# Kernel optimization log

Measured on AMD Instinct MI355X. Metric: run time of the kernel, lower is better.

## Reference

```python
import jax, jax.numpy as jnp
import numpy as np

N_NODES = 262144
N_EDGES = 4194304
N_GRAPHS = 1024
IN_DIM = 10
HIDDEN = 32


def setup_inputs() -> dict:
    key = jax.random.key(0)
    ks = jax.random.split(key, 8)
    x = jax.random.normal(ks[0], (N_NODES, IN_DIM), dtype=jnp.float32)
    edge_index = jax.random.randint(ks[1], (2, N_EDGES), 0, N_NODES, dtype=jnp.int64)
    batch = jnp.sort(jax.random.randint(ks[2], (N_NODES,), 0, N_GRAPHS, dtype=jnp.int64))
    W1 = jax.random.normal(ks[3], (IN_DIM, HIDDEN), dtype=jnp.float32) * (1.0 / np.sqrt(IN_DIM))
    b1 = jnp.zeros((HIDDEN,), dtype=jnp.float32)
    W2 = jax.random.normal(ks[4], (HIDDEN, HIDDEN), dtype=jnp.float32) * (1.0 / np.sqrt(HIDDEN))
    b2 = jnp.zeros((HIDDEN,), dtype=jnp.float32)
    Wlin = jax.random.normal(ks[5], (HIDDEN, 1), dtype=jnp.float32) * (1.0 / np.sqrt(HIDDEN))
    blin = jnp.zeros((1,), dtype=jnp.float32)
    return {"x": x, "edge_index": edge_index, "batch": batch,
            "W1": W1, "b1": b1, "W2": W2, "b2": b2, "Wlin": Wlin, "blin": blin}


def _gcn_norm(edge_index, num_nodes):
    # PyG GCNConv default: add self-loops, symmetric normalization.
    loop = jnp.arange(num_nodes, dtype=edge_index.dtype)
    src = jnp.concatenate([edge_index[0], loop])
    dst = jnp.concatenate([edge_index[1], loop])
    deg = jax.ops.segment_sum(jnp.ones_like(dst, dtype=jnp.float32), dst,
                              num_segments=num_nodes)
    dinv = jnp.where(deg > 0, jax.lax.rsqrt(deg), 0.0)
    norm = dinv[src] * dinv[dst]  # [E+N]
    return src, dst, norm


def _gcn_conv(x, W, b, src, dst, norm, num_nodes):
    h = x @ W                              # [N, out]
    msg = h[src] * norm[:, None]           # gather + scale  [E+N, out]
    out = jax.ops.segment_sum(msg, dst, num_segments=num_nodes)  # scatter-add
    return out + b


def reference(x, edge_index, batch, W1, b1, W2, b2, Wlin, blin):
    n = x.shape[0]
    src, dst, norm = _gcn_norm(edge_index, n)
    h = jax.nn.relu(_gcn_conv(x, W1, b1, src, dst, norm, n))
    h = jax.nn.relu(_gcn_conv(h, W2, b2, src, dst, norm, n))
    # global_mean_pool over graph ids
    sums = jax.ops.segment_sum(h, batch, num_segments=N_GRAPHS)
    cnt = jax.ops.segment_sum(jnp.ones((n,), dtype=h.dtype), batch,
                              num_segments=N_GRAPHS)
    pooled = sums / jnp.maximum(cnt, 1.0)[:, None]   # [G, hidden]
    return (pooled @ Wlin + blin).squeeze(-1)        # [G]
```

## Files before the change

kernel.cpp:

```cpp
#include <hip/hip_runtime.h>
#include <stdint.h>

#define N_NODES 262144
#define N_EDGES 4194304
#define N_GRAPHS 1024
#define IN_DIM 10
#define HIDDEN 32
#define NBUCKET 1024
#define NSUB 8
#define CAP_SUB 704
#define BROW (NSUB * CAP_SUB)
#define STG_CAP BROW
#define S_EDGES 16384
#define PA_BLOCKS (N_EDGES / S_EDGES)
#define PA_THREADS 512

__device__ __forceinline__ float fatomic_add(float* p, float v) {
    return unsafeAtomicAdd(p, v);
}

__device__ __forceinline__ uint16_t f2bf(float f) {
    uint32_t u = __float_as_uint(f);
    u = (u + 0x7FFF + ((u >> 16) & 1)) >> 16;
    return (uint16_t)u;
}
__device__ __forceinline__ float bf_lo(uint32_t w) { return __uint_as_float(w << 16); }
__device__ __forceinline__ float bf_hi(uint32_t w) { return __uint_as_float(w & 0xFFFF0000u); }


__global__ __launch_bounds__(PA_THREADS) void passA(const int* __restrict__ src,
                                                    const int* __restrict__ dst,
                                                    int* __restrict__ bcnt,
                                                    uint32_t* __restrict__ arena) {
    __shared__ int hist[NBUCKET];
    __shared__ int cur[NBUCKET];
    int blk = blockIdx.x, t = threadIdx.x;
    int j = blk & (NSUB - 1);
    size_t e0 = (size_t)blk * S_EDGES;

    for (int k = t; k < NBUCKET; k += PA_THREADS) hist[k] = 0;
    __syncthreads();

    const int4* dp = reinterpret_cast<const int4*>(dst + e0);
    const int4* sp = reinterpret_cast<const int4*>(src + e0);

    for (int k = t; k < S_EDGES / 4; k += PA_THREADS) {
        int4 d4 = dp[k];
        atomicAdd(&hist[d4.x >> 8], 1);
        atomicAdd(&hist[d4.y >> 8], 1);
        atomicAdd(&hist[d4.z >> 8], 1);
        atomicAdd(&hist[d4.w >> 8], 1);
    }
    __syncthreads();

    for (int k = t; k < NBUCKET; k += PA_THREADS) {
        int h = hist[k];
        cur[k] = (h > 0) ? atomicAdd(&bcnt[(k * NSUB + j) * 16], h) : 0;
    }
    __syncthreads();

    for (int k = t; k < S_EDGES / 4; k += PA_THREADS) {
        int4 d4 = dp[k];
        int4 s4 = sp[k];
        {
            int d = d4.x, b = d >> 8;
            int pos = atomicAdd(&cur[b], 1);
            if (pos < CAP_SUB)
                arena[(size_t)(b * NSUB + j) * CAP_SUB + pos] = ((uint32_t)(d & 255) << 18) | (uint32_t)s4.x;
        }
        {
            int d = d4.y, b = d >> 8;
            int pos = atomicAdd(&cur[b], 1);
            if (pos < CAP_SUB)
                arena[(size_t)(b * NSUB + j) * CAP_SUB + pos] = ((uint32_t)(d & 255) << 18) | (uint32_t)s4.y;
        }
        {
            int d = d4.z, b = d >> 8;
            int pos = atomicAdd(&cur[b], 1);
            if (pos < CAP_SUB)
                arena[(size_t)(b * NSUB + j) * CAP_SUB + pos] = ((uint32_t)(d & 255) << 18) | (uint32_t)s4.z;
        }
        {
            int d = d4.w, b = d >> 8;
            int pos = atomicAdd(&cur[b], 1);
            if (pos < CAP_SUB)
                arena[(size_t)(b * NSUB + j) * CAP_SUB + pos] = ((uint32_t)(d & 255) << 18) | (uint32_t)s4.w;
        }
    }
}


__global__ void bucket_sort(uint32_t* __restrict__ arena, const int* __restrict__ bcnt,
                            const float* __restrict__ x, float* __restrict__ dinv,
                            uint32_t* __restrict__ binfo, uint16_t* __restrict__ xs) {
    __shared__ uint32_t stg[STG_CAP];
    __shared__ int scnt[NSUB];
    __shared__ int h[256];
    __shared__ int cur[256];
    __shared__ float dsh[256];
    int b = blockIdx.x, t = threadIdx.x;
    int base = b * 256;
    if (t < NSUB) {
        int c = bcnt[(b * NSUB + t) * 16];
        scnt[t] = (c > CAP_SUB) ? CAP_SUB : c;
    }
    h[t] = 0;
    __syncthreads();
    int off = 0;
    #pragma unroll
    for (int j = 0; j < NSUB; ++j) {
        int len = scnt[j];
        const uint32_t* sp = arena + (size_t)(b * NSUB + j) * CAP_SUB;
        for (int k = t; k < len; k += 256) stg[off + k] = sp[k];
        off += len;
    }
    int nb = off;
    __syncthreads();
    for (int k = t; k < nb; k += 256) atomicAdd(&h[stg[k] >> 18], 1);
    __syncthreads();
    int myh = h[t];
    #pragma unroll
    for (int o = 1; o < 256; o <<= 1) {
        int v = (t >= o) ? h[t - o] : 0;
        __syncthreads();
        h[t] += v;
        __syncthreads();
    }
    int excl = h[t] - myh;
    binfo[base + t] = ((uint32_t)excl << 13) | (uint32_t)myh;
    float dv = rsqrtf(1.0f + (float)myh);
    dinv[base + t] = dv;
    dsh[t] = dv;
    cur[t] = excl;
    __syncthreads();
    uint32_t* wp = arena + (size_t)b * BROW;
    for (int k = t; k < nb; k += 256) {
        uint32_t w = stg[k];
        int d = w >> 18;
        int pos = atomicAdd(&cur[d], 1);
        wp[pos] = w & 0x3FFFF;
    }
    for (int idx = t; idx < 256 * 16; idx += 256) {
        int n = idx >> 4, k = idx & 15;
        float val = (k < IN_DIM) ? x[(size_t)(base + n) * IN_DIM + k] * dsh[n] : 0.0f;
        xs[(size_t)(base + n) * 16 + k] = f2bf(val);
    }
}


__global__ void agg1(const uint16_t* __restrict__ xs, const uint32_t* __restrict__ arena,
                     const uint32_t* __restrict__ binfo, float* __restrict__ aggx) {
    int lane = threadIdx.x & 63;
    int wid = (blockIdx.x * 256 + threadIdx.x) >> 6;
    int n = wid * 16 + (lane >> 2);
    int q = lane & 1, g = (lane >> 1) & 1;
    uint32_t info = binfo[n];
    int beg = (int)(info >> 13), len = (int)(info & 0x1FFF);
    const uint32_t* ep = arena + (size_t)(n >> 8) * BROW + beg;
    const uint4* Xv = reinterpret_cast<const uint4*>(xs);
    float a[8];
    #pragma unroll
    for (int j = 0; j < 8; ++j) a[j] = 0.0f;
    if (g == 0) {
        uint4 v = Xv[(size_t)n * 2 + q];
        a[0] += bf_lo(v.x); a[1] += bf_hi(v.x);
        a[2] += bf_lo(v.y); a[3] += bf_hi(v.y);
        a[4] += bf_lo(v.z); a[5] += bf_hi(v.z);
        a[6] += bf_lo(v.w); a[7] += bf_hi(v.w);
    }
    for (int i = g; i < len; i += 2) {
        int si = (int)ep[i];
        uint4 v = Xv[(size_t)si * 2 + q];
        a[0] += bf_lo(v.x); a[1] += bf_hi(v.x);
        a[2] += bf_lo(v.y); a[3] += bf_hi(v.y);
        a[4] += bf_lo(v.z); a[5] += bf_hi(v.z);
        a[6] += bf_lo(v.w); a[7] += bf_hi(v.w);
    }
    #pragma unroll
    for (int j = 0; j < 8; ++j) a[j] += __shfl_xor(a[j], 2);
    if (g == 0) {
        float4* p = reinterpret_cast<float4*>(aggx + (size_t)n * 12);
        if (q == 0) {
            p[0] = make_float4(a[0], a[1], a[2], a[3]);
            p[1] = make_float4(a[4], a[5], a[6], a[7]);
        } else {
            p[2] = make_float4(a[0], a[1], a[2], a[3]);
        }
    }
}


__global__ void dense1(const float* __restrict__ aggx, const float* __restrict__ W1,
                       const float* __restrict__ dinv, const float* __restrict__ b1,
                       uint16_t* __restrict__ zs) {
    __shared__ float w[IN_DIM * HIDDEN];
    __shared__ float zt[8][12];
    int t = threadIdx.x;
    for (int j = t; j < IN_DIM * HIDDEN; j += 256) w[j] = W1[j];
    int base = blockIdx.x * 8;
    if (t < 96) zt[t / 12][t % 12] = aggx[(size_t)base * 12 + t];
    __syncthreads();
    int i = t >> 5, c = t & 31;
    int n = base + i;
    float s = 0.0f;
    #pragma unroll
    for (int k = 0; k < IN_DIM; ++k) s += zt[i][k] * w[k * HIDDEN + c];
    float dn = dinv[n];
    zs[(size_t)n * HIDDEN + c] = f2bf(fmaxf(dn * s + b1[c], 0.0f) * dn);
}


__global__ void agg2(const uint16_t* __restrict__ zs, const uint32_t* __restrict__ arena,
                     const uint32_t* __restrict__ binfo, float* __restrict__ aggz) {
    int lane = threadIdx.x & 63;
    int wid = (blockIdx.x * 256 + threadIdx.x) >> 6;
    int n = wid * 16 + (lane >> 2);
    int q = lane & 3;
    uint32_t info = binfo[n];
    int beg = (int)(info >> 13), len = (int)(info & 0x1FFF);
    const uint32_t* ep = arena + (size_t)(n >> 8) * BROW + beg;
    const uint4* Zv = reinterpret_cast<const uint4*>(zs);
    float a[8];
    {
        uint4 v = Zv[(size_t)n * 4 + q];
        a[0] = bf_lo(v.x); a[1] = bf_hi(v.x);
        a[2] = bf_lo(v.y); a[3] = bf_hi(v.y);
        a[4] = bf_lo(v.z); a[5] = bf_hi(v.z);
        a[6] = bf_lo(v.w); a[7] = bf_hi(v.w);
    }
    for (int i = 0; i < len; ++i) {
        int si = (int)ep[i];
        uint4 v = Zv[(size_t)si * 4 + q];
        a[0] += bf_lo(v.x); a[1] += bf_hi(v.x);
        a[2] += bf_lo(v.y); a[3] += bf_hi(v.y);
        a[4] += bf_lo(v.z); a[5] += bf_hi(v.z);
        a[6] += bf_lo(v.w); a[7] += bf_hi(v.w);
    }
    float4* p = reinterpret_cast<float4*>(aggz + (size_t)n * 32 + q * 8);
    p[0] = make_float4(a[0], a[1], a[2], a[3]);
    p[1] = make_float4(a[4], a[5], a[6], a[7]);
}


__global__ void dense2_pool(const float* __restrict__ aggz, const float* __restrict__ W2,
                            const float* __restrict__ dinv, const float* __restrict__ b2,
                            const int* __restrict__ batch, float* __restrict__ pooled) {
    __shared__ float w[HIDDEN * HIDDEN];
    __shared__ float zt[8][HIDDEN];
    __shared__ float vsh[8][HIDDEN + 1];
    __shared__ int bsh[8];
    int t = threadIdx.x;
    for (int j = t; j < HIDDEN * HIDDEN; j += 256) w[j] = W2[j];
    int base = blockIdx.x * 8;
    zt[t >> 5][t & 31] = aggz[(size_t)base * HIDDEN + t];
    if (t < 8) bsh[t] = batch[base + t];
    __syncthreads();
    int i = t >> 5, c = t & 31;
    int n = base + i;
    float s = 0.0f;
    #pragma unroll
    for (int k = 0; k < HIDDEN; ++k) s += zt[i][k] * w[k * HIDDEN + c];
    vsh[i][c] = fmaxf(dinv[n] * s + b2[c], 0.0f);
    __syncthreads();
    if (t < HIDDEN) {
        float run = vsh[0][t];
        int cur = bsh[0];
        #pragma unroll
        for (int j = 1; j < 8; ++j) {
            int bg = bsh[j];
            if (bg == cur) run += vsh[j][t];
            else {
                fatomic_add(&pooled[(size_t)cur * HIDDEN + t], run);
                run = vsh[j][t];
                cur = bg;
            }
        }
        fatomic_add(&pooled[(size_t)cur * HIDDEN + t], run);
    }
}


__global__ void final_k(const float* __restrict__ pooled, const int* __restrict__ batch,
                        const float* __restrict__ Wlin, const float* __restrict__ blin,
                        float* __restrict__ out) {
    int g = blockIdx.x * blockDim.x + threadIdx.x;
    if (g < N_GRAPHS) {
        int lo = 0, hi = N_NODES;
        while (lo < hi) { int mid = (lo + hi) >> 1; if (batch[mid] < g) lo = mid + 1; else hi = mid; }
        int first = lo;
        lo = 0; hi = N_NODES;
        while (lo < hi) { int mid = (lo + hi) >> 1; if (batch[mid] <= g) lo = mid + 1; else hi = mid; }
        float cc = (float)(lo - first);
        if (cc < 1.0f) cc = 1.0f;
        float s = 0.0f;
        #pragma unroll
        for (int c = 0; c < HIDDEN; ++c) s += pooled[(size_t)g * HIDDEN + c] * Wlin[c];
        out[g] = s / cc + blin[0];
    }
}


extern "C" void kernel_launch(void* const* d_in, const int* in_sizes, int n_in,
                              void* d_out, int out_size, void* d_ws, size_t ws_size,
                              hipStream_t stream) {
    const float* x     = (const float*)d_in[0];
    const int*   ei    = (const int*)d_in[1];
    const int*   batch = (const int*)d_in[2];
    const float* W1    = (const float*)d_in[3];
    const float* b1    = (const float*)d_in[4];
    const float* W2    = (const float*)d_in[5];
    const float* b2    = (const float*)d_in[6];
    const float* Wlin  = (const float*)d_in[7];
    const float* blin  = (const float*)d_in[8];
    float* out = (float*)d_out;

    const int* src = ei;
    const int* dst = ei + N_EDGES;

    const size_t N = N_NODES;
    float*    F      = (float*)d_ws;
    uint16_t* zs     = (uint16_t*)F;
    uint16_t* xs     = (uint16_t*)(F + 8 * N);
    float*    aggx   = F + 16 * N;
    float*    aggz   = F + 28 * N;
    float*    dinv   = F + 60 * N;
    uint32_t* binfo  = (uint32_t*)(dinv + N);
    int*      bcnt   = (int*)(binfo + N);
    float*    pooled = (float*)(bcnt + NBUCKET * NSUB * 16);
    uint32_t* arena  = (uint32_t*)(pooled + (size_t)N_GRAPHS * HIDDEN);

    size_t zbytes = ((size_t)NBUCKET * NSUB * 16 + (size_t)N_GRAPHS * HIDDEN) * sizeof(int);
    hipMemsetAsync(bcnt, 0, zbytes, stream);

    passA<<<PA_BLOCKS, PA_THREADS, 0, stream>>>(src, dst, bcnt, arena);
    bucket_sort<<<NBUCKET, 256, 0, stream>>>(arena, bcnt, x, dinv, binfo, xs);
    agg1<<<N_NODES / 64, 256, 0, stream>>>(xs, arena, binfo, aggx);
    dense1<<<N_NODES / 8, 256, 0, stream>>>(aggx, W1, dinv, b1, zs);
    agg2<<<N_NODES / 64, 256, 0, stream>>>(zs, arena, binfo, aggz);
    dense2_pool<<<N_NODES / 8, 256, 0, stream>>>(aggz, W2, dinv, b2, batch, pooled);
    final_k<<<(N_GRAPHS + 255) / 256, 256, 0, stream>>>(pooled, batch, Wlin, blin, out);
}
```

Baseline: 306.3 us.

## Fuse neighbor aggregation with dense transforms and pooling per 64-node block

```diff
diff --git a/kernel.cpp b/kernel.cpp
--- a/kernel.cpp
+++ b/kernel.cpp
@@ -148,11 +148,19 @@
 }
 
 
-__global__ void agg1(const uint16_t* __restrict__ xs, const uint32_t* __restrict__ arena,
-                     const uint32_t* __restrict__ binfo, float* __restrict__ aggx) {
-    int lane = threadIdx.x & 63;
-    int wid = (blockIdx.x * 256 + threadIdx.x) >> 6;
-    int n = wid * 16 + (lane >> 2);
+__global__ void agg1_dense1(const uint16_t* __restrict__ xs, const uint32_t* __restrict__ arena,
+                            const uint32_t* __restrict__ binfo, const float* __restrict__ dinv,
+                            const float* __restrict__ W1, const float* __restrict__ b1,
+                            uint16_t* __restrict__ zs) {
+    __shared__ float ash[64 * 12];
+    __shared__ float w[IN_DIM * HIDDEN];
+    int t = threadIdx.x;
+    int base = blockIdx.x * 64;
+    for (int j = t; j < IN_DIM * HIDDEN; j += 256) w[j] = W1[j];
+
+    int lane = t & 63;
+    int nib = (t >> 6) * 16 + (lane >> 2);
+    int n = base + nib;
     int q = lane & 1, g = (lane >> 1) & 1;
     uint32_t info = binfo[n];
     int beg = (int)(info >> 13), len = (int)(info & 0x1FFF);
@@ -179,42 +187,55 @@
     #pragma unroll
     for (int j = 0; j < 8; ++j) a[j] += __shfl_xor(a[j], 2);
     if (g == 0) {
-        float4* p = reinterpret_cast<float4*>(aggx + (size_t)n * 12);
         if (q == 0) {
-            p[0] = make_float4(a[0], a[1], a[2], a[3]);
-            p[1] = make_float4(a[4], a[5], a[6], a[7]);
+            #pragma unroll
+            for (int j = 0; j < 8; ++j) ash[nib * 12 + j] = a[j];
         } else {
-            p[2] = make_float4(a[0], a[1], a[2], a[3]);
-        }
-    }
-}
-
-
-__global__ void dense1(const float* __restrict__ aggx, const float* __restrict__ W1,
-                       const float* __restrict__ dinv, const float* __restrict__ b1,
-                       uint16_t* __restrict__ zs) {
-    __shared__ float w[IN_DIM * HIDDEN];
-    __shared__ float zt[8][12];
+            #pragma unroll
+            for (int j = 0; j < 4; ++j) ash[nib * 12 + 8 + j] = a[j];
+        }
+    }
+    __syncthreads();
+
+    int dn_i = t >> 2, c0 = (t & 3) * 8;
+    int node = base + dn_i;
+    float s[8];
+    #pragma unroll
+    for (int j = 0; j < 8; ++j) s[j] = 0.0f;
+    #pragma unroll
+    for (int k = 0; k < IN_DIM; ++k) {
+        float ak = ash[dn_i * 12 + k];
+        #pragma unroll
+        for (int j = 0; j < 8; ++j) s[j] += ak * w[k * HIDDEN + c0 + j];
+    }
+    float dv = dinv[node];
+    uint32_t pk[4];
+    #pragma unroll
+    for (int j = 0; j < 4; ++j) {
+        float v0 = fmaxf(dv * s[2 * j] + b1[c0 + 2 * j], 0.0f) * dv;
+        float v1 = fmaxf(dv * s[2 * j + 1] + b1[c0 + 2 * j + 1], 0.0f) * dv;
+        pk[j] = (uint32_t)f2bf(v0) | ((uint32_t)f2bf(v1) << 16);
+    }
+    reinterpret_cast<uint4*>(zs)[(size_t)node * 4 + (t & 3)] =
+        make_uint4(pk[0], pk[1], pk[2], pk[3]);
+}
+
+
+__global__ void agg2_dense2_pool(const uint16_t* __restrict__ zs, const uint32_t* __restrict__ arena,
+                                 const uint32_t* __restrict__ binfo, const float* __restrict__ dinv,
+                                 const float* __restrict__ W2, const float* __restrict__ b2,
+                                 const int* __restrict__ batch, float* __restrict__ pooled) {
+    __shared__ float vsh[64 * 33];
+    __shared__ float w[HIDDEN * HIDDEN];
+    __shared__ int bsh[64];
     int t = threadIdx.x;
-    for (int j = t; j < IN_DIM * HIDDEN; j += 256) w[j] = W1[j];
-    int base = blockIdx.x * 8;
-    if (t < 96) zt[t / 12][t % 12] = aggx[(size_t)base * 12 + t];
-    __syncthreads();
-    int i = t >> 5, c = t & 31;
-    int n = base + i;
-    float s = 0.0f;
-    #pragma unroll
-    for (int k = 0; k < IN_DIM; ++k) s += zt[i][k] * w[k * HIDDEN + c];
-    float dn = dinv[n];
-    zs[(size_t)n * HIDDEN + c] = f2bf(fmaxf(dn * s + b1[c], 0.0f) * dn);
-}
-
-
-__global__ void agg2(const uint16_t* __restrict__ zs, const uint32_t* __restrict__ arena,
-                     const uint32_t* __restrict__ binfo, float* __restrict__ aggz) {
-    int lane = threadIdx.x & 63;
-    int wid = (blockIdx.x * 256 + threadIdx.x) >> 6;
-    int n = wid * 16 + (lane >> 2);
+    int base = blockIdx.x * 64;
+    for (int j = t; j < HIDDEN * HIDDEN; j += 256) w[j] = W2[j];
+    if (t < 64) bsh[t] = batch[base + t];
+
+    int lane = t & 63;
+    int nib = (t >> 6) * 16 + (lane >> 2);
+    int n = base + nib;
     int q = lane & 3;
     uint32_t info = binfo[n];
     int beg = (int)(info >> 13), len = (int)(info & 0x1FFF);
@@ -236,47 +257,46 @@
         a[4] += bf_lo(v.z); a[5] += bf_hi(v.z);
         a[6] += bf_lo(v.w); a[7] += bf_hi(v.w);
     }
-    float4* p = reinterpret_cast<float4*>(aggz + (size_t)n * 32 + q * 8);
-    p[0] = make_float4(a[0], a[1], a[2], a[3]);
-    p[1] = make_float4(a[4], a[5], a[6], a[7]);
-}
-
-
-__global__ void dense2_pool(const float* __restrict__ aggz, const float* __restrict__ W2,
-                            const float* __restrict__ dinv, const float* __restrict__ b2,
-                            const int* __restrict__ batch, float* __restrict__ pooled) {
-    __shared__ float w[HIDDEN * HIDDEN];
-    __shared__ float zt[8][HIDDEN];
-    __shared__ float vsh[8][HIDDEN + 1];
-    __shared__ int bsh[8];
-    int t = threadIdx.x;
-    for (int j = t; j < HIDDEN * HIDDEN; j += 256) w[j] = W2[j];
-    int base = blockIdx.x * 8;
-    zt[t >> 5][t & 31] = aggz[(size_t)base * HIDDEN + t];
-    if (t < 8) bsh[t] = batch[base + t];
-    __syncthreads();
-    int i = t >> 5, c = t & 31;
-    int n = base + i;
-    float s = 0.0f;
-    #pragma unroll
-    for (int k = 0; k < HIDDEN; ++k) s += zt[i][k] * w[k * HIDDEN + c];
-    vsh[i][c] = fmaxf(dinv[n] * s + b2[c], 0.0f);
-    __syncthreads();
-    if (t < HIDDEN) {
-        float run = vsh[0][t];
-        int cur = bsh[0];
+    #pragma unroll
+    for (int j = 0; j < 8; ++j) vsh[nib * 33 + q * 8 + j] = a[j];
+    __syncthreads();
+
+    int dn_i = t >> 2, c0 = (t & 3) * 8;
+    int node = base + dn_i;
+    float s[8];
+    #pragma unroll
+    for (int j = 0; j < 8; ++j) s[j] = 0.0f;
+    #pragma unroll
+    for (int k = 0; k < HIDDEN; ++k) {
+        float ak = vsh[dn_i * 33 + k];
         #pragma unroll
-        for (int j = 1; j < 8; ++j) {
-            int bg = bsh[j];
-            if (bg == cur) run += vsh[j][t];
-            else {
-                fatomic_add(&pooled[(size_t)cur * HIDDEN + t], run);
-                run = vsh[j][t];
-                cur = bg;
-            }
-        }
-        fatomic_add(&pooled[(size_t)cur * HIDDEN + t], run);
-    }
+        for (int j = 0; j < 8; ++j) s[j] += ak * w[k * HIDDEN + c0 + j];
+    }
+    float dv = dinv[node];
+    float v[8];
+    #pragma unroll
+    for (int j = 0; j < 8; ++j) v[j] = fmaxf(dv * s[j] + b2[c0 + j], 0.0f);
+    __syncthreads();
+    #pragma unroll
+    for (int j = 0; j < 8; ++j) vsh[dn_i * 33 + c0 + j] = v[j];
+    __syncthreads();
+
+    int col = t & 31, seg = t >> 5;
+    int r0 = seg * 8;
+    float run = vsh[r0 * 33 + col];
+    int cur = bsh[r0];
+    #pragma unroll
+    for (int j = 1; j < 8; ++j) {
+        int bg = bsh[r0 + j];
+        float vv = vsh[(r0 + j) * 33 + col];
+        if (bg == cur) run += vv;
+        else {
+            fatomic_add(&pooled[(size_t)cur * HIDDEN + col], run);
+            run = vv;
+            cur = bg;
+        }
+    }
+    fatomic_add(&pooled[(size_t)cur * HIDDEN + col], run);
 }
 
 
@@ -321,9 +341,7 @@
     float*    F      = (float*)d_ws;
     uint16_t* zs     = (uint16_t*)F;
     uint16_t* xs     = (uint16_t*)(F + 8 * N);
-    float*    aggx   = F + 16 * N;
-    float*    aggz   = F + 28 * N;
-    float*    dinv   = F + 60 * N;
+    float*    dinv   = F + 16 * N;
     uint32_t* binfo  = (uint32_t*)(dinv + N);
     int*      bcnt   = (int*)(binfo + N);
     float*    pooled = (float*)(bcnt + NBUCKET * NSUB * 16);
@@ -334,9 +352,7 @@
 
     passA<<<PA_BLOCKS, PA_THREADS, 0, stream>>>(src, dst, bcnt, arena);
     bucket_sort<<<NBUCKET, 256, 0, stream>>>(arena, bcnt, x, dinv, binfo, xs);
-    agg1<<<N_NODES / 64, 256, 0, stream>>>(xs, arena, binfo, aggx);
-    dense1<<<N_NODES / 8, 256, 0, stream>>>(aggx, W1, dinv, b1, zs);
-    agg2<<<N_NODES / 64, 256, 0, stream>>>(zs, arena, binfo, aggz);
-    dense2_pool<<<N_NODES / 8, 256, 0, stream>>>(aggz, W2, dinv, b2, batch, pooled);
+    agg1_dense1<<<N_NODES / 64, 256, 0, stream>>>(xs, arena, binfo, dinv, W1, b1, zs);
+    agg2_dense2_pool<<<N_NODES / 64, 256, 0, stream>>>(zs, arena, binfo, dinv, W2, b2, batch, pooled);
     final_k<<<(N_GRAPHS + 255) / 256, 256, 0, stream>>>(pooled, batch, Wlin, blin, out);
 }
```

Measured after the change: 248.8 us. 18.7% less time.
